# Kernel tuning notes

Measured on AMD Instinct MI355X. Metric: run time of the kernel, lower is better.

Reference implementation:

```python
import jax, jax.numpy as jnp
import numpy as np

SAMPLE = 16          # init kwarg `sample`
DILATED_RATE = 2     # init kwarg `dilated_rate`
RADIUS = 16.0        # hardcoded in forward: ball_query(16, ...)
NSAMPLE = SAMPLE * DILATED_RATE
XYZ_SCALE = 30.0     # spread points so radius-16 ball is a real neighborhood


def setup_inputs() -> dict:
    key = jax.random.key(0)
    k1, k2 = jax.random.split(key)
    xyz = jax.random.normal(k1, (4, 4096, 3), dtype=jnp.float32) * XYZ_SCALE
    feature = jax.random.normal(k2, (4, 4096, 64), dtype=jnp.float32)
    return {"xyz": xyz, "feature": feature}


def _ball_query(xyz, radius, nsample):
    """pointnet2-style ball query: for each point, the first `nsample` point
    indices (in ascending index order) with squared distance < radius^2;
    rows with fewer than nsample hits are padded with the first hit.
    xyz: [B,N,3] -> idx int32 [B,N,nsample]."""
    B, N, _ = xyz.shape
    sq = jnp.sum(xyz * xyz, axis=-1)                                   # [B,N]
    d2 = sq[:, :, None] + sq[:, None, :] - 2.0 * jnp.einsum(
        'bnd,bmd->bnm', xyz, xyz)                                      # [B,N,N]
    in_ball = d2 < (radius * radius)
    # score = N - j for in-ball points, 0 otherwise; top_k then returns the
    # smallest in-ball indices j, already sorted ascending in j.
    col_score = (N - jnp.arange(N, dtype=jnp.int32))[None, None, :]
    score = jnp.where(in_ball, col_score, 0)                           # [B,N,N]
    vals, idx = jax.lax.top_k(score, nsample)                          # [B,N,K]
    first = idx[..., 0:1]
    return jnp.where(vals > 0, idx, first)                             # pad with first hit


def _group(points, idx):
    """grouping_operation: points [B,N,C] (channel-last), idx [B,N,K] ->
    grouped [B,C,N,K]."""
    gathered = jax.vmap(lambda p, i: p[i])(points, idx)  # [B,N,K,C]
    return gathered.transpose(0, 3, 1, 2)                # [B,C,N,K]


def reference(xyz, feature):
    ids = _ball_query(xyz, RADIUS, NSAMPLE)              # [B,N,NSAMPLE]
    center = ids[:, :, 0:1]
    if DILATED_RATE == 1:
        dilated_ids = ids[:, :, :SAMPLE]
    else:
        region = ids[:, :, (DILATED_RATE - 1) * SAMPLE: DILATED_RATE * SAMPLE - 1]
        dilated_ids = jnp.concatenate([center, region], axis=-1)  # [B,N,SAMPLE]
    dilated_xyz = _group(xyz, dilated_ids)          # [B,3,N,SAMPLE]
    dilated_feature = _group(feature, dilated_ids)  # [B,C,N,SAMPLE]
    return (dilated_xyz, dilated_feature)
```

## Files before the change

### kernel.cpp

```cpp
#include <hip/hip_runtime.h>


#define BB 4
#define NN 4096
#define KK 16
#define PLANE (NN * KK)
#define NC 20
#define NCELL2 (NC * NC)

__device__ __forceinline__ int cell1d(float v)
{
    int c = (int)floorf((v + 160.0f) * 0.0625f);
    c = c < 0 ? 0 : c;
    return c > (NC - 1) ? (NC - 1) : c;
}

__global__ __launch_bounds__(256)
void preprocess(const float* __restrict__ xyz, float4* __restrict__ P,
                float4* __restrict__ SP, int* __restrict__ CS)
{
#pragma clang fp contract(off)
    __shared__ int hist[NCELL2];
    __shared__ int wsum[4];

    const int b = blockIdx.x;
    const int t = threadIdx.x;
    const int lane = t & 63, wave = t >> 6;
    const float* xb = xyz + b * NN * 3;

    if (t < NCELL2) hist[t] = 0;
    if (t + 256 < NCELL2) hist[t + 256] = 0;
    __syncthreads();

    for (int i = t; i < NN; i += 256) {
        const float x = xb[3 * i], y = xb[3 * i + 1], z = xb[3 * i + 2];
        const float sq = (x * x + y * y) + z * z;
        P[(b << 12) + i] = make_float4(x, y, z, sq);
        const int c = cell1d(y) * NC + cell1d(x);
        atomicAdd(&hist[c], 1);
    }
    __syncthreads();

    const int c0 = t * 2;
    const int c1 = (c0 + 2 < NCELL2) ? c0 + 2 : NCELL2;
    int s = 0;
    for (int c = c0; c < c1; ++c) s += hist[c];
    int x = s;
#pragma unroll
    for (int off = 1; off < 64; off <<= 1) {
        const int u = __shfl_up(x, off, 64);
        if (lane >= off) x += u;
    }
    if (lane == 63) wsum[wave] = x;
    __syncthreads();
    int wb = 0;
    for (int w = 0; w < wave; ++w) wb += wsum[w];
    int acc = wb + x - s;

    int* cs = CS + b * (NCELL2 + 1);
    for (int c = c0; c < c1; ++c) {
        const int v = hist[c];
        cs[c]   = acc;
        hist[c] = acc;
        acc += v;
    }
    if (t == 0) cs[NCELL2] = NN;
    __syncthreads();

    for (int i = t; i < NN; i += 256) {
        const float x = xb[3 * i], y = xb[3 * i + 1], z = xb[3 * i + 2];
        const int c = cell1d(y) * NC + cell1d(x);
        const int slot = atomicAdd(&hist[c], 1);
        SP[(b << 12) + slot] = make_float4(x, y, z, __int_as_float(i));
    }
}

__global__ __launch_bounds__(256, 4)
void query_gather(const float4* __restrict__ P, const float4* __restrict__ SP,
                  const int* __restrict__ CS, const float* __restrict__ feat,
                  float* __restrict__ out)
{
#pragma clang fp contract(off)
    __shared__ unsigned int mask[4][128];
    __shared__ int sids[4 * KK];

    const int beta = blockIdx.x;
    const int b    = beta >> 10;
    const int p0   = (beta & 1023) * 4;
    const int t    = threadIdx.x;
    const int lane = t & 63;
    const int wave = t >> 6;

    const float4* Pb  = P  + (b << 12);
    const float4* Sb  = SP + (b << 12);
    const int*    csb = CS + b * (NCELL2 + 1);

    const float4 pi  = Pb[p0 + wave];
    const float  sqi = pi.w;

    unsigned int* m = mask[wave];
    m[2 * lane]     = 0u;
    m[2 * lane + 1] = 0u;

    {
        const int cx = cell1d(pi.x), cy = cell1d(pi.y);
        const int xlo = cx > 0 ? cx - 1 : 0;
        const int xhi = cx < NC - 1 ? cx + 1 : NC - 1;
#pragma unroll
        for (int rr = 0; rr < 3; ++rr) {
            int yy = cy + rr - 1;
            yy = yy < 0 ? 0 : (yy > NC - 1 ? NC - 1 : yy);
            const int cb = yy * NC;
            const int s  = csb[cb + xlo];
            const int e  = csb[cb + xhi + 1];
            for (int v = s + lane; v < e; v += 64) {
                const float4 a = Sb[v];
                const float sqj = (a.x * a.x + a.y * a.y) + a.z * a.z;
                const float dot = (pi.x * a.x + pi.y * a.y) + pi.z * a.z;
                const float d2  = (sqi + sqj) - 2.0f * dot;
                if (d2 < 256.0f) {
                    const int j = __float_as_int(a.w);
                    atomicOr(&m[j >> 5], 1u << (j & 31));
                }
            }
        }
    }

    {
        const unsigned int lo  = m[2 * lane];
        const unsigned int hiw = m[2 * lane + 1];
        const unsigned long long w = ((unsigned long long)hiw << 32) | lo;
        const int c = __popcll(w);
        int x = c;
#pragma unroll
        for (int off = 1; off < 64; off <<= 1) {
            const int u = __shfl_up(x, off, 64);
            if (lane >= off) x += u;
        }
        const int cnt  = __shfl(x, 63, 64);
        const int base = x - c;

        int fj = 0x7fffffff;
        if (w) fj = (lane << 6) + __builtin_ctzll(w);
        for (int off = 32; off; off >>= 1) {
            const int o = __shfl_xor(fj, off, 64);
            fj = fj < o ? fj : o;
        }

        int* row = sids + wave * KK;
        if (w && base <= 30 && base + c > 16) {
            unsigned long long ww = w;
            int r = base;
            while (ww) {
                if (r > 30) break;
                if (r >= 16) row[r - 15] = (lane << 6) + __builtin_ctzll(ww);
                ww &= ww - 1;
                ++r;
            }
        }
        const int hi = (cnt < 31 ? cnt : 31) - 16;
        if (lane < KK && (lane == 0 || lane > hi)) row[lane] = fj;
    }
    __syncthreads();

    const int rowi = t & 63;
    const int part = t >> 6;
    const int id   = sids[rowi];
    const int ob   = (beta & 1023) * 64 + rowi;

    if (part == 0) {
        const float4 p = Pb[id];
        float* o0 = out + (size_t)b * 3 * PLANE + ob;
        o0[0]         = p.x;
        o0[PLANE]     = p.y;
        o0[2 * PLANE] = p.z;
    }

    const float4* frow = reinterpret_cast<const float4*>(feat + ((size_t)(b << 12) + id) * 64) + part * 4;
    float* o1 = out + (size_t)BB * 3 * PLANE + (size_t)b * 64 * PLANE
                    + (size_t)(part * 16) * PLANE + ob;
#pragma unroll
    for (int q = 0; q < 4; ++q) {
        const float4 v = frow[q];
        float* oc = o1 + (size_t)(4 * q) * PLANE;
        oc[0]         = v.x;
        oc[PLANE]     = v.y;
        oc[2 * PLANE] = v.z;
        oc[3 * PLANE] = v.w;
    }
}

extern "C" void kernel_launch(void* const* d_in, const int* in_sizes, int n_in,
                              void* d_out, int out_size, void* d_ws, size_t ws_size,
                              hipStream_t stream) {
    const float* xyz  = (const float*)d_in[0];
    const float* feat = (const float*)d_in[1];
    float* out = (float*)d_out;

    char* ws = (char*)d_ws;
    float4* P  = (float4*)(ws);
    float4* SP = (float4*)(ws + 262144);
    int*    CS = (int*)   (ws + 524288);

    preprocess  <<<BB,          256, 0, stream>>>(xyz, P, SP, CS);
    query_gather<<<BB * NN / 4, 256, 0, stream>>>(P, SP, CS, feat, out);
}
```

Baseline: 114.1 us.

## Widen preprocess to 1024 threads, drop P buffer, read xyz directly

The preprocess kernel now runs 1024 threads per batch. Each thread loads four points with three float4 loads and keeps them in registers across the histogram, a single-wave 64-lane scan and the scatter, so xyz is read once instead of twice. The intermediate P array (xyz plus squared norm) is removed. query_gather now reads the query point and the gathered output coordinates directly from the strided xyz input and recomputes the squared norm. This shortens the serial 4-block preprocess stage at the cost of unaligned scalar loads in the gather kernel.

Measured after the change: 107.1 us. 1.07x faster.

```diff
diff --git a/kernel.cpp b/kernel.cpp
--- a/kernel.cpp
+++ b/kernel.cpp
@@ -15,68 +15,82 @@
     return c > (NC - 1) ? (NC - 1) : c;
 }
 
-__global__ __launch_bounds__(256)
-void preprocess(const float* __restrict__ xyz, float4* __restrict__ P,
-                float4* __restrict__ SP, int* __restrict__ CS)
+__global__ __launch_bounds__(1024)
+void preprocess(const float* __restrict__ xyz, float4* __restrict__ SP,
+                int* __restrict__ CS)
 {
 #pragma clang fp contract(off)
     __shared__ int hist[NCELL2];
-    __shared__ int wsum[4];
 
     const int b = blockIdx.x;
     const int t = threadIdx.x;
-    const int lane = t & 63, wave = t >> 6;
-    const float* xb = xyz + b * NN * 3;
+    const float4* xb4 = (const float4*)(xyz + (size_t)b * NN * 3);
 
     if (t < NCELL2) hist[t] = 0;
-    if (t + 256 < NCELL2) hist[t + 256] = 0;
-    __syncthreads();
-
-    for (int i = t; i < NN; i += 256) {
-        const float x = xb[3 * i], y = xb[3 * i + 1], z = xb[3 * i + 2];
-        const float sq = (x * x + y * y) + z * z;
-        P[(b << 12) + i] = make_float4(x, y, z, sq);
-        const int c = cell1d(y) * NC + cell1d(x);
-        atomicAdd(&hist[c], 1);
-    }
-    __syncthreads();
-
-    const int c0 = t * 2;
-    const int c1 = (c0 + 2 < NCELL2) ? c0 + 2 : NCELL2;
-    int s = 0;
-    for (int c = c0; c < c1; ++c) s += hist[c];
-    int x = s;
-#pragma unroll
-    for (int off = 1; off < 64; off <<= 1) {
-        const int u = __shfl_up(x, off, 64);
-        if (lane >= off) x += u;
-    }
-    if (lane == 63) wsum[wave] = x;
-    __syncthreads();
-    int wb = 0;
-    for (int w = 0; w < wave; ++w) wb += wsum[w];
-    int acc = wb + x - s;
-
-    int* cs = CS + b * (NCELL2 + 1);
-    for (int c = c0; c < c1; ++c) {
-        const int v = hist[c];
-        cs[c]   = acc;
-        hist[c] = acc;
-        acc += v;
-    }
-    if (t == 0) cs[NCELL2] = NN;
-    __syncthreads();
-
-    for (int i = t; i < NN; i += 256) {
-        const float x = xb[3 * i], y = xb[3 * i + 1], z = xb[3 * i + 2];
-        const int c = cell1d(y) * NC + cell1d(x);
-        const int slot = atomicAdd(&hist[c], 1);
-        SP[(b << 12) + slot] = make_float4(x, y, z, __int_as_float(i));
+    __syncthreads();
+
+    const float4 v0 = xb4[3 * t];
+    const float4 v1 = xb4[3 * t + 1];
+    const float4 v2 = xb4[3 * t + 2];
+    const float px0 = v0.x, py0 = v0.y, pz0 = v0.z;
+    const float px1 = v0.w, py1 = v1.x, pz1 = v1.y;
+    const float px2 = v1.z, py2 = v1.w, pz2 = v2.x;
+    const float px3 = v2.y, py3 = v2.z, pz3 = v2.w;
+    const int c0 = cell1d(py0) * NC + cell1d(px0);
+    const int c1 = cell1d(py1) * NC + cell1d(px1);
+    const int c2 = cell1d(py2) * NC + cell1d(px2);
+    const int c3 = cell1d(py3) * NC + cell1d(px3);
+    atomicAdd(&hist[c0], 1);
+    atomicAdd(&hist[c1], 1);
+    atomicAdd(&hist[c2], 1);
+    atomicAdd(&hist[c3], 1);
+    __syncthreads();
+
+    if (t < 64) {
+        const int base = t * 7;
+        int loc0 = 0, loc1 = 0, loc2 = 0, loc3 = 0, loc4 = 0, loc5 = 0, loc6 = 0;
+        if (base + 0 < NCELL2) loc0 = hist[base + 0];
+        if (base + 1 < NCELL2) loc1 = hist[base + 1];
+        if (base + 2 < NCELL2) loc2 = hist[base + 2];
+        if (base + 3 < NCELL2) loc3 = hist[base + 3];
+        if (base + 4 < NCELL2) loc4 = hist[base + 4];
+        if (base + 5 < NCELL2) loc5 = hist[base + 5];
+        if (base + 6 < NCELL2) loc6 = hist[base + 6];
+        const int s = loc0 + loc1 + loc2 + loc3 + loc4 + loc5 + loc6;
+        int x = s;
+#pragma unroll
+        for (int off = 1; off < 64; off <<= 1) {
+            const int u = __shfl_up(x, off, 64);
+            if (t >= off) x += u;
+        }
+        int acc = x - s;
+        int* cs = CS + b * (NCELL2 + 1);
+        if (base + 0 < NCELL2) { cs[base + 0] = acc; hist[base + 0] = acc; acc += loc0; }
+        if (base + 1 < NCELL2) { cs[base + 1] = acc; hist[base + 1] = acc; acc += loc1; }
+        if (base + 2 < NCELL2) { cs[base + 2] = acc; hist[base + 2] = acc; acc += loc2; }
+        if (base + 3 < NCELL2) { cs[base + 3] = acc; hist[base + 3] = acc; acc += loc3; }
+        if (base + 4 < NCELL2) { cs[base + 4] = acc; hist[base + 4] = acc; acc += loc4; }
+        if (base + 5 < NCELL2) { cs[base + 5] = acc; hist[base + 5] = acc; acc += loc5; }
+        if (base + 6 < NCELL2) { cs[base + 6] = acc; hist[base + 6] = acc; acc += loc6; }
+        if (t == 0) cs[NCELL2] = NN;
+    }
+    __syncthreads();
+
+    {
+        int slot;
+        slot = atomicAdd(&hist[c0], 1);
+        SP[(b << 12) + slot] = make_float4(px0, py0, pz0, __int_as_float(4 * t + 0));
+        slot = atomicAdd(&hist[c1], 1);
+        SP[(b << 12) + slot] = make_float4(px1, py1, pz1, __int_as_float(4 * t + 1));
+        slot = atomicAdd(&hist[c2], 1);
+        SP[(b << 12) + slot] = make_float4(px2, py2, pz2, __int_as_float(4 * t + 2));
+        slot = atomicAdd(&hist[c3], 1);
+        SP[(b << 12) + slot] = make_float4(px3, py3, pz3, __int_as_float(4 * t + 3));
     }
 }
 
 __global__ __launch_bounds__(256, 4)
-void query_gather(const float4* __restrict__ P, const float4* __restrict__ SP,
+void query_gather(const float* __restrict__ xyz, const float4* __restrict__ SP,
                   const int* __restrict__ CS, const float* __restrict__ feat,
                   float* __restrict__ out)
 {
@@ -91,19 +105,22 @@
     const int lane = t & 63;
     const int wave = t >> 6;
 
-    const float4* Pb  = P  + (b << 12);
+    const float* xb   = xyz + (size_t)b * NN * 3;
     const float4* Sb  = SP + (b << 12);
     const int*    csb = CS + b * (NCELL2 + 1);
 
-    const float4 pi  = Pb[p0 + wave];
-    const float  sqi = pi.w;
+    const int   ip  = p0 + wave;
+    const float pix = xb[3 * ip];
+    const float piy = xb[3 * ip + 1];
+    const float piz = xb[3 * ip + 2];
+    const float sqi = (pix * pix + piy * piy) + piz * piz;
 
     unsigned int* m = mask[wave];
     m[2 * lane]     = 0u;
     m[2 * lane + 1] = 0u;
 
     {
-        const int cx = cell1d(pi.x), cy = cell1d(pi.y);
+        const int cx = cell1d(pix), cy = cell1d(piy);
         const int xlo = cx > 0 ? cx - 1 : 0;
         const int xhi = cx < NC - 1 ? cx + 1 : NC - 1;
 #pragma unroll
@@ -116,7 +133,7 @@
             for (int v = s + lane; v < e; v += 64) {
                 const float4 a = Sb[v];
                 const float sqj = (a.x * a.x + a.y * a.y) + a.z * a.z;
-                const float dot = (pi.x * a.x + pi.y * a.y) + pi.z * a.z;
+                const float dot = (pix * a.x + piy * a.y) + piz * a.z;
                 const float d2  = (sqi + sqj) - 2.0f * dot;
                 if (d2 < 256.0f) {
                     const int j = __float_as_int(a.w);
@@ -169,11 +186,10 @@
     const int ob   = (beta & 1023) * 64 + rowi;
 
     if (part == 0) {
-        const float4 p = Pb[id];
         float* o0 = out + (size_t)b * 3 * PLANE + ob;
-        o0[0]         = p.x;
-        o0[PLANE]     = p.y;
-        o0[2 * PLANE] = p.z;
+        o0[0]         = xb[3 * id];
+        o0[PLANE]     = xb[3 * id + 1];
+        o0[2 * PLANE] = xb[3 * id + 2];
     }
 
     const float4* frow = reinterpret_cast<const float4*>(feat + ((size_t)(b << 12) + id) * 64) + part * 4;
@@ -198,10 +214,9 @@
     float* out = (float*)d_out;
 
     char* ws = (char*)d_ws;
-    float4* P  = (float4*)(ws);
-    float4* SP = (float4*)(ws + 262144);
-    int*    CS = (int*)   (ws + 524288);
-
-    preprocess  <<<BB,          256, 0, stream>>>(xyz, P, SP, CS);
-    query_gather<<<BB * NN / 4, 256, 0, stream>>>(P, SP, CS, feat, out);
-}
+    float4* SP = (float4*)(ws);
+    int*    CS = (int*)   (ws + 262144);
+
+    preprocess  <<<BB,          1024, 0, stream>>>(xyz, SP, CS);
+    query_gather<<<BB * NN / 4, 256,  0, stream>>>(xyz, SP, CS, feat, out);
+}
```
